# Kernel tuning notes

Hardware: AMD Instinct MI355X
Metric: run time of the kernel (lower is better)

The kernel has to match this reference:

```python
import jax, jax.numpy as jnp
import numpy as np

B, E, W, HID, HOR = 16, 128, 256, 64, 12
EPS = 1e-5


def conv1d(x, w, b, stride=1, padding=0, groups=1):
    # x: [N, Cin, L], w: [Cout, Cin//groups, K]
    y = jax.lax.conv_general_dilated(x, w, (stride,), [(padding, padding)],
                                     feature_group_count=groups,
                                     dimension_numbers=('NCH', 'OIH', 'NCH'))
    return y + b[None, :, None]


def setup_inputs() -> dict:
    key = jax.random.key(0)
    ks = jax.random.split(key, 20)
    def rn(k, shape, scale):
        return jax.random.normal(k, shape, dtype=jnp.float32) * scale
    return {
        'x': rn(ks[0], (B, 1, W), 1.0),
        'noise': rn(ks[1], (HOR, B * E), 1.0),
        'affine_weight': jnp.ones((E,), jnp.float32),
        'affine_bias': jnp.zeros((E,), jnp.float32),
        'pe_w1': rn(ks[2], (32, 1, 5), 1.0 / np.sqrt(5.0)),
        'pe_b1': jnp.zeros((32,), jnp.float32),
        'bn_gamma': jnp.ones((32,), jnp.float32),
        'bn_beta': jnp.zeros((32,), jnp.float32),
        'bn_mean': jnp.zeros((32,), jnp.float32),
        'bn_var': jnp.ones((32,), jnp.float32),
        'pe_w2': rn(ks[3], (E, 32, 1), 1.0 / np.sqrt(32.0)),
        'pe_b2': jnp.zeros((E,), jnp.float32),
        'net_w1': rn(ks[4], (E, 64, 1, 2), 1.0 / np.sqrt(2.0)),
        'net_b1': jnp.zeros((E, 64), jnp.float32),
        'net_w2': rn(ks[5], (E, 64, 4, 2), 1.0 / np.sqrt(8.0)),
        'net_b2': jnp.zeros((E, 64), jnp.float32),
        'net_w3': rn(ks[6], (E, 1, 64, 1), 1.0 / np.sqrt(64.0)),
        'net_b3': jnp.zeros((E, 1), jnp.float32),
        'gat_wl': rn(ks[7], (HID, HID), 1.0 / np.sqrt(HID)),
        'gat_bl': jnp.zeros((HID,), jnp.float32),
        'gat_wr': rn(ks[8], (HID, HID), 1.0 / np.sqrt(HID)),
        'gat_br': jnp.zeros((HID,), jnp.float32),
        'gat_attn': rn(ks[9], (HID,), 1.0 / np.sqrt(HID)),
        'out_w': rn(ks[10], (E, HID), 1.0 / np.sqrt(HID)),
        'out_b': jnp.zeros((E,), jnp.float32),
        'ce_w': rn(ks[11], (HID, 3), 1.0 / np.sqrt(3.0)),
        'ce_b': jnp.zeros((HID,), jnp.float32),
        'cd_w': rn(ks[12], (4, HID), 1.0 / np.sqrt(HID)),
        'cd_b': jnp.zeros((4,), jnp.float32),
        'q_w': rn(ks[13], (32, W), 1.0 / np.sqrt(W)),
        'q_b': jnp.zeros((32,), jnp.float32),
        'k_w': rn(ks[14], (32, W), 1.0 / np.sqrt(W)),
        'k_b': jnp.zeros((32,), jnp.float32),
    }


def reference(x, noise, affine_weight, affine_bias, pe_w1, pe_b1, bn_gamma, bn_beta,
              bn_mean, bn_var, pe_w2, pe_b2, net_w1, net_b1, net_w2, net_b2, net_w3,
              net_b3, gat_wl, gat_bl, gat_wr, gat_br, gat_attn, out_w, out_b,
              ce_w, ce_b, cd_w, cd_b, q_w, q_b, k_w, k_b):
    # instance norm over time axis (unbiased=False, no eps, as in the torch code)
    mean = jnp.mean(x, axis=2, keepdims=True)              # [B,1,1]
    std = jnp.sqrt(jnp.var(x, axis=2, keepdims=True))
    xn = (x - mean) / std

    # path_encoder: conv(1->32,k5,p2) + ReLU + BN(eval) + conv(32->E,k1)
    h0 = jax.nn.relu(conv1d(xn, pe_w1, pe_b1, padding=2))
    h0 = (h0 - bn_mean[None, :, None]) / jnp.sqrt(bn_var + EPS)[None, :, None]
    h0 = h0 * bn_gamma[None, :, None] + bn_beta[None, :, None]
    xf = conv1d(h0, pe_w2, pe_b2)                          # [B,E,W]
    xf = xf * affine_weight[None, :, None] + affine_bias[None, :, None]

    # adjacency learner: softmax(Q K^T) over nodes, then hard threshold
    q = jnp.einsum('bew,hw->beh', xf, q_w) + q_b           # [B,E,32]
    k = jnp.einsum('bew,hw->beh', xf, k_w) + k_b
    adj_soft = jax.nn.softmax(jnp.einsum('bih,bjh->bij', q, k), axis=-1)  # [B,E,E]
    adj_bin = (adj_soft > 0.5).astype(jnp.float32)

    def cnn1d(xc, w1, b1, w2, b2, w3, b3):
        # xc: [B,1,W] -> [B,1,HID]; kernel=stride=down_factor//2=2
        h1 = jnp.tanh(conv1d(xc, w1, b1, stride=2))
        h2 = jnp.tanh(conv1d(h1, w2, b2, stride=2, groups=16))
        return jnp.tanh(conv1d(h2, w3, b3))

    vcnn = jax.vmap(cnn1d, in_axes=(0, 0, 0, 0, 0, 0, 0))

    def gat(h, adj):
        # GATv2, single head, is_concat: e[b,i,j] = a^T lrelu(g_r[i]+g_l[j])
        gl = jnp.einsum('bnf,of->bno', h, gat_wl) + gat_bl   # [B,N,HID]
        gr = jnp.einsum('bnf,of->bno', h, gat_wr) + gat_br
        gs = gr[:, :, None, :] + gl[:, None, :, :]           # [B,N,N,HID]
        e = jnp.einsum('bijf,f->bij', jax.nn.leaky_relu(gs, 0.2), gat_attn)
        e = jnp.where(adj == 0, jnp.float32(-1e20), e)
        a = jax.nn.softmax(e, axis=2)
        return jnp.einsum('bij,bjf->bif', a, gr)             # [B,N,HID]

    def mech(Q_t, P_t, adj, nz):
        Hh, Ee, Vv = Q_t[:, 0], Q_t[:, 1], Q_t[:, 2]
        al, be, ga, et = P_t[:, 0], P_t[:, 1], P_t[:, 2], P_t[:, 3]
        E_coup = jnp.einsum('bij,bj->bi', adj, Ee.reshape(B, E)).reshape(B * E)
        H_new = Hh - al * Hh
        E_new = Ee + be * Hh - ga * Ee + 0.1 * E_coup
        V_new = Vv + et * Ee + nz * 0.01
        return jnp.stack([H_new, E_new, V_new], axis=1)

    Q0 = jnp.tile(jnp.array([1.0, 0.0, 0.0], jnp.float32), (B * E, 1))

    def step(carry, nz):
        xc, Q_t = carry
        xper = xc.transpose(1, 0, 2)[:, :, None, :]          # [E,B,1,W]
        h = vcnn(xper, net_w1, net_b1, net_w2, net_b2, net_w3, net_b3)
        h = h[:, :, 0, :].transpose(1, 0, 2)                 # [B,E,HID]
        h_temp = gat(h, adj_bin)
        H_causal = jnp.tanh(Q_t @ ce_w.T + ce_b).reshape(B, E, HID)
        h = h + jnp.tanh(h_temp) + H_causal
        x_pred = jnp.einsum('beh,eh->be', h, out_w) + out_b  # grouped conv == per-node dot
        x_new = jnp.concatenate([xc[:, :, 1:], x_pred[:, :, None]], axis=2)
        P_t = jax.nn.sigmoid(h.reshape(B * E, HID) @ cd_w.T + cd_b)
        Q_new = mech(Q_t, P_t, adj_bin, nz)
        return (x_new, Q_new), (x_pred, P_t)

    (_, Q_final), (x_preds, P_all) = jax.lax.scan(step, (xf, Q0), noise)
    x_pred_all = x_preds.transpose(1, 2, 0)                  # [B,E,HOR]
    out = (x_pred_all - affine_bias[None, :, None]) / affine_weight[None, :, None]
    out = out * std + mean
    return out, Q_final.reshape(B, E, 3), P_all[-1].reshape(B, E, 4), adj_soft
```

## Files before the change

kernel.cpp:

```cpp
#include <hip/hip_runtime.h>


typedef __attribute__((ext_vector_type(4))) float f32x4;

struct Params {
  const float *__restrict__ x, *__restrict__ noise, *__restrict__ aw, *__restrict__ ab,
              *__restrict__ pe_w1, *__restrict__ pe_b1, *__restrict__ bn_g, *__restrict__ bn_b,
              *__restrict__ bn_m, *__restrict__ bn_v, *__restrict__ pe_w2, *__restrict__ pe_b2,
              *__restrict__ w1, *__restrict__ b1, *__restrict__ w2, *__restrict__ b2,
              *__restrict__ w3, *__restrict__ b3, *__restrict__ wl, *__restrict__ bl,
              *__restrict__ wr, *__restrict__ br, *__restrict__ attn, *__restrict__ out_w,
              *__restrict__ out_b, *__restrict__ ce_w, *__restrict__ ce_b, *__restrict__ cd_w,
              *__restrict__ cd_b, *__restrict__ q_w, *__restrict__ q_b, *__restrict__ k_w,
              *__restrict__ k_b;
  float* ws;
  float* out;
};

__device__ __forceinline__ float fast_tanh(float x) {
  float t = exp2f(fminf(2.8853900818f * x, 126.0f));
  return 1.0f - 2.0f * __builtin_amdgcn_rcpf(t + 1.0f);
}
__device__ __forceinline__ float fast_sigmoid(float x) {
  float t = exp2f(fminf(-1.44269504f * x, 126.0f));
  return __builtin_amdgcn_rcpf(1.0f + t);
}
__device__ __forceinline__ float wsum(float v) {
  #pragma unroll
  for (int m = 1; m < 64; m <<= 1) v += __shfl_xor(v, m, 64);
  return v;
}
__device__ __forceinline__ float wmax(float v) {
  #pragma unroll
  for (int m = 1; m < 64; m <<= 1) v = fmaxf(v, __shfl_xor(v, m, 64));
  return v;
}
__device__ __forceinline__ float load_llc(const float* p) {
  return __hip_atomic_load(p, __ATOMIC_RELAXED, __HIP_MEMORY_SCOPE_AGENT);
}
__device__ __forceinline__ void store_llc(float* p, float v) {
  __hip_atomic_store(p, v, __ATOMIC_RELAXED, __HIP_MEMORY_SCOPE_AGENT);
}
__device__ __forceinline__ f32x4 load_llc4(const float* p) {
  f32x4 v;
  asm volatile("global_load_dwordx4 %0, %1, off sc0 sc1" : "=v"(v) : "v"(p));
  return v;
}
__device__ __forceinline__ unsigned to_bf16(float f) {
  unsigned u = __float_as_uint(f);
  return (u + 0x7fffu + ((u >> 16) & 1u)) >> 16;
}
__device__ __forceinline__ unsigned pk(float lo, float hi) {
  return to_bf16(lo) | (to_bf16(hi) << 16);
}
__device__ __forceinline__ float blo(unsigned w) { return __uint_as_float(w << 16); }
__device__ __forceinline__ float bhi(unsigned w) { return __uint_as_float(w & 0xffff0000u); }

#define OFF_MS   0
#define OFF_EB   32
#define OFF_CNT  4128
#define OFF_QV   16416
#define OFF_KV   81952
#define OFF_GL   147488
#define OFF_GR   409632
#define OFF_H0   671776
#define OFF_XW   802848
#define OFF_G    1359904
#define OFF_ADJ  1916960

__global__ __launch_bounds__(256)
void k1_h0(Params P) {
  __shared__ float red[8];
  const int tid = threadIdx.x, blk = blockIdx.x;
  const int idx = blk * 256 + tid;
  const int b = idx >> 13, c = (idx >> 8) & 31, w = idx & 255;
  const int lane = tid & 63, wv = tid >> 6;

  float v = P.x[b * 256 + w];
  float s = wsum(v), s2 = wsum(v * v);
  if (lane == 0) { red[wv] = s; red[4 + wv] = s2; }
  __syncthreads();
  float st  = red[0] + red[1] + red[2] + red[3];
  float st2 = red[4] + red[5] + red[6] + red[7];
  float mean = st * (1.f / 256.f);
  float var  = st2 * (1.f / 256.f) - mean * mean;
  float sd   = sqrtf(var);
  float* ms = P.ws + OFF_MS;
  if (tid == 0) { ms[b] = mean; ms[16 + b] = sd; }

  float rstd = 1.f / sd;
  float acc = P.pe_b1[c];
  #pragma unroll
  for (int k = 0; k < 5; k++) {
    int u = w - 2 + k;
    float xv = (u >= 0 && u < 256) ? (P.x[b * 256 + u] - mean) * rstd : 0.f;
    acc += P.pe_w1[c * 5 + k] * xv;
  }
  acc = fmaxf(acc, 0.f);
  float sc = P.bn_g[c] / sqrtf(P.bn_v[c] + 1e-5f);
  (P.ws + OFF_H0)[idx] = (acc - P.bn_m[c]) * sc + P.bn_b[c];
}

__global__ __launch_bounds__(256)
void k2_xf(Params P) {
  const int idx = blockIdx.x * 256 + threadIdx.x;
  const int b = idx >> 15, e = (idx >> 8) & 127, w = idx & 255;
  const float* w2p  = P.pe_w2 + e * 32;
  const float* hcol = P.ws + OFF_H0 + b * 8192 + w;
  float acc = P.pe_b2[e];
  #pragma unroll 8
  for (int c = 0; c < 32; c++) acc += w2p[c] * hcol[c * 256];
  acc = acc * P.aw[e] + P.ab[e];
  (P.ws + OFF_XW)[(b * 128 + e) * 272 + w] = acc;
}

__global__ __launch_bounds__(256)
void k34(Params P) {
  if (blockIdx.x < 2048) {
    const int row = blockIdx.x;
    const int es  = row & 127;
    const int s   = threadIdx.x;
    const float* w1p = P.w1 + es * 128;
    const float* w2p = P.w2 + es * 512;
    const float* w3p = P.w3 + es * 64;
    const float* b1p = P.b1 + es * 64;
    const float* b2p = P.b2 + es * 64;
    const float  b3v = P.b3[es];
    const float* xr  = P.ws + OFF_XW + row * 272;
    if (s >= 253) return;
    float X0 = xr[s], X1 = xr[s + 1], X2 = xr[s + 2], X3 = xr[s + 3];
    float acc = 0.f;
    #pragma unroll 1
    for (int g2 = 0; g2 < 16; g2++) {
      float h1v[8];
      #pragma unroll
      for (int ic = 0; ic < 4; ic++) {
        int ch = g2 * 4 + ic;
        float ww0 = w1p[ch * 2], ww1 = w1p[ch * 2 + 1], bb = b1p[ch];
        h1v[ic * 2 + 0] = fast_tanh(bb + ww0 * X0 + ww1 * X1);
        h1v[ic * 2 + 1] = fast_tanh(bb + ww0 * X2 + ww1 * X3);
      }
      #pragma unroll
      for (int oc = 0; oc < 4; oc++) {
        int ch = g2 * 4 + oc;
        const float* wq = w2p + ch * 8;
        float a2 = b2p[ch];
        #pragma unroll
        for (int u = 0; u < 8; u++) a2 += wq[u] * h1v[u];
        acc += w3p[ch] * fast_tanh(a2);
      }
    }
    (P.ws + OFF_G)[row * 272 + s] = fast_tanh(b3v + acc);
  } else {
    const int gtid = (blockIdx.x - 2048) * 256 + threadIdx.x;
    if (gtid < 16) ((int*)(P.ws + OFF_CNT))[gtid * 32] = 0;
    const int half = gtid >> 16;
    const int idx  = gtid & 65535;
    const int row  = idx >> 5, h = idx & 31;
    const float* wm  = half ? P.k_w : P.q_w;
    const float* bv  = half ? P.k_b : P.q_b;
    const float* xr  = P.ws + OFF_XW + row * 272;
    const float* wrw = wm + h * 256;
    float acc = bv[h];
    #pragma unroll 8
    for (int w = 0; w < 256; w += 4) {
      float4 xx = *(const float4*)(xr + w);
      float4 wq = *(const float4*)(wrw + w);
      acc += xx.x * wq.x + xx.y * wq.y + xx.z * wq.z + xx.w * wq.w;
    }
    ((half ? P.ws + OFF_KV : P.ws + OFF_QV))[idx] = acc;
  }
}

__global__ __launch_bounds__(256)
void k5_adj(Params P) {
  __shared__ __align__(16) float hbuf[4 * 64];
  const int tid = threadIdx.x, lane = tid & 63, wv = tid >> 6;
  const int row = blockIdx.x * 4 + wv;
  const int b = row >> 7;
  float* ws = P.ws;
  float* hb = hbuf + wv * 64;
  unsigned char* adjb = (unsigned char*)(ws + OFF_ADJ);

  if (lane < 32) hb[lane] = (ws + OFF_QV)[row * 32 + lane];
  __syncthreads();
  float ev0, ev1;
  #pragma unroll
  for (int half = 0; half < 2; half++) {
    int j = lane + half * 64;
    const float* kr = ws + OFF_KV + (b * 128 + j) * 32;
    float acc = 0.f;
    #pragma unroll
    for (int h = 0; h < 32; h += 4) {
      float4 kk = *(const float4*)(kr + h);
      float4 qq = *(const float4*)(hb + h);
      acc += qq.x * kk.x + qq.y * kk.y + qq.z * kk.z + qq.w * kk.w;
    }
    if (half == 0) ev0 = acc; else ev1 = acc;
  }
  float m   = wmax(fmaxf(ev0, ev1));
  float p0  = __expf(ev0 - m), p1 = __expf(ev1 - m);
  float inv = 1.f / wsum(p0 + p1);
  float a0 = p0 * inv, a1 = p1 * inv;
  P.out[38912 + row * 128 + lane]      = a0;
  P.out[38912 + row * 128 + lane + 64] = a1;
  adjb[row * 128 + lane]      = (a0 > 0.5f) ? 1 : 0;
  adjb[row * 128 + lane + 64] = (a1 > 0.5f) ? 1 : 0;
}

__global__ __launch_bounds__(1024, 4)
void k_scan(Params P) {
  __shared__ __align__(16) unsigned glS2_[4096];
  __shared__ __align__(16) unsigned grTS_[4096];
  __shared__ __align__(16) unsigned WS_[4096];
  __shared__ __align__(16) float wscb[16 * 336];
  __shared__ __align__(16) float attnS[64];
  const int tid = threadIdx.x, lane = tid & 63, wv = tid >> 6;
  const int row = blockIdx.x * 16 + wv;
  const int b = row >> 7, e = row & 127;
  float* ws = P.ws;
  float* abuf = wscb + wv * 336;
  float* hb   = abuf + 128;
  float* h1b  = abuf + 192;
  float* hist = abuf + 320;
  const float4* hb4   = (const float4*)hb;
  const float4* abuf4 = (const float4*)abuf;
  const float4* attn4 = (const float4*)attnS;
  char* glS  = (char*)glS2_;
  char* grTS = (char*)grTS_;
  char* WSc  = (char*)WS_;
  const float* grow_G = ws + OFF_G + row * 272;
  const unsigned char* arow = (const unsigned char*)(ws + OFF_ADJ) + row * 128;
  int* cntb = (int*)(ws + OFF_CNT) + b * 32;

  {
    int o = tid >> 4, c = tid & 15;
    float4 vl = *(const float4*)(P.wl + o * 64 + c * 4);
    float4 vr = *(const float4*)(P.wr + o * 64 + c * 4);
    uint4 u;
    u.x = pk(vl.x, vr.x); u.y = pk(vl.y, vr.y);
    u.z = pk(vl.z, vr.z); u.w = pk(vl.w, vr.w);
    *(uint4*)(WSc + o * 256 + ((c ^ (o & 15)) << 4)) = u;
  }
  if (tid < 64) attnS[tid] = P.attn[tid];

  float cew0 = P.ce_w[lane * 3], cew1 = P.ce_w[lane * 3 + 1], cew2 = P.ce_w[lane * 3 + 2];
  float cebv = P.ce_b[lane];
  float cdw0 = P.cd_w[lane], cdw1 = P.cd_w[64 + lane], cdw2 = P.cd_w[128 + lane], cdw3 = P.cd_w[192 + lane];
  float cdb0 = P.cd_b[0], cdb1 = P.cd_b[1], cdb2 = P.cd_b[2], cdb3 = P.cd_b[3];
  float outw = P.out_w[e * 64 + lane], outb = P.out_b[e];
  float blv = P.bl[lane], brv = P.br[lane];
  float awv = P.aw[e], abv = P.ab[e];
  float meanb = ws[OFF_MS + b], stdb = ws[OFF_MS + 16 + b];
  float w10 = P.w1[e * 128 + lane * 2], w11 = P.w1[e * 128 + lane * 2 + 1];
  float b1v = P.b1[e * 64 + lane], b2v = P.b2[e * 64 + lane];
  float w3v = P.w3[e * 64 + lane], b3c = P.b3[e];
  float w2r[8];
  {
    const float4* w24 = (const float4*)(P.w2 + e * 512 + lane * 8);
    float4 a = w24[0], c = w24[1];
    w2r[0] = a.x; w2r[1] = a.y; w2r[2] = a.z; w2r[3] = a.w;
    w2r[4] = c.x; w2r[5] = c.y; w2r[6] = c.z; w2r[7] = c.w;
  }
  const bool a0b = arow[lane] != 0, a1b = arow[lane + 64] != 0;
  float h_own = grow_G[4 * lane];
  float xA = (ws + OFF_XW)[row * 272 + 253];
  float xB = (ws + OFF_XW)[row * 272 + 254];
  float xC = (ws + OFF_XW)[row * 272 + 255];
  float q0 = 1.f, q1 = 0.f, q2 = 0.f;
  if (lane == 0) store_llc(ws + OFF_EB + row, 0.f);

  __syncthreads();

  hb[lane] = h_own;
  __syncthreads();
  float gri;
  {
    float glx = blv, grx = brv;
    const int k = lane & 15;
    #pragma unroll
    for (int q = 0; q < 16; q++) {
      float4 hq = hb4[q];
      uint4 w = *(const uint4*)(WSc + lane * 256 + ((q ^ k) << 4));
      glx += hq.x * blo(w.x) + hq.y * blo(w.y) + hq.z * blo(w.z) + hq.w * blo(w.w);
      grx += hq.x * bhi(w.x) + hq.y * bhi(w.y) + hq.z * bhi(w.z) + hq.w * bhi(w.w);
    }
    store_llc(ws + OFF_GL + row * 64 + lane, glx);
    store_llc(ws + OFF_GR + b * 8192 + lane * 128 + e, grx);
    gri = grx;
  }

  const int pp = tid >> 4, pc = tid & 15;
  const int ff = tid >> 4, fc = tid & 15;

  #pragma unroll 1
  for (int t = 0; t < 12; t++) {
    asm volatile("s_waitcnt vmcnt(0)" ::: "memory");
    __syncthreads();
    if (tid == 0) {
      __hip_atomic_fetch_add(cntb, 1, __ATOMIC_RELAXED, __HIP_MEMORY_SCOPE_AGENT);
      const int target = (t + 1) * 8;
      while (__hip_atomic_load(cntb, __ATOMIC_RELAXED, __HIP_MEMORY_SCOPE_AGENT) < target)
        __builtin_amdgcn_s_sleep(2);
    }
    __syncthreads();

    const float* glG   = ws + OFF_GL + (t & 1) * 131072 + b * 8192;
    const float* grTG  = ws + OFF_GR + (t & 1) * 131072 + b * 8192;
    const float* EbO   = ws + OFF_EB + (t & 1) * 2048;
    float*       EbN   = ws + OFF_EB + ((t + 1) & 1) * 2048;
    float*       glGn  = ws + OFF_GL + ((t + 1) & 1) * 131072;
    float*       grTGn = ws + OFF_GR + ((t + 1) & 1) * 131072;

    {
      f32x4 va = load_llc4(glG + pp * 64 + pc * 4);
      f32x4 vb = load_llc4(glG + (pp + 64) * 64 + pc * 4);
      f32x4 vc = load_llc4(grTG + ff * 128 + fc * 8);
      f32x4 vd = load_llc4(grTG + ff * 128 + fc * 8 + 4);
      asm volatile("s_waitcnt vmcnt(0)" ::: "memory");
      __builtin_amdgcn_sched_barrier(0);
      uint4 ug;
      ug.x = pk(va[0], vb[0]); ug.y = pk(va[1], vb[1]);
      ug.z = pk(va[2], vb[2]); ug.w = pk(va[3], vb[3]);
      *(uint4*)(glS + pp * 256 + ((pc ^ (pp & 15)) << 4)) = ug;
      uint4 ur;
      ur.x = pk(vc[0], vc[1]); ur.y = pk(vc[2], vc[3]);
      ur.z = pk(vd[0], vd[1]); ur.w = pk(vd[2], vd[3]);
      *(uint4*)(grTS + ff * 256 + ((fc ^ (ff & 15)) << 4)) = ur;
    }
    hb[lane] = gri;
    __syncthreads();

    float ev0 = 0.f, ev1 = 0.f;
    {
      const char* r0 = glS + lane * 256;
      const int k = lane & 15;
      #pragma unroll
      for (int c = 0; c < 16; c++) {
        float4 hq = hb4[c];
        float4 aq = attn4[c];
        uint4 g = *(const uint4*)(r0 + ((c ^ k) << 4));
        float v;
        v = hq.x + blo(g.x); ev0 += fmaxf(v, 0.2f * v) * aq.x;
        v = hq.x + bhi(g.x); ev1 += fmaxf(v, 0.2f * v) * aq.x;
        v = hq.y + blo(g.y); ev0 += fmaxf(v, 0.2f * v) * aq.y;
        v = hq.y + bhi(g.y); ev1 += fmaxf(v, 0.2f * v) * aq.y;
        v = hq.z + blo(g.z); ev0 += fmaxf(v, 0.2f * v) * aq.z;
        v = hq.z + bhi(g.z); ev1 += fmaxf(v, 0.2f * v) * aq.z;
        v = hq.w + blo(g.w); ev0 += fmaxf(v, 0.2f * v) * aq.w;
        v = hq.w + bhi(g.w); ev1 += fmaxf(v, 0.2f * v) * aq.w;
      }
    }
    ev0 = a0b ? ev0 : -1e20f;
    ev1 = a1b ? ev1 : -1e20f;
    float m   = wmax(fmaxf(ev0, ev1));
    float p0  = __expf(ev0 - m), p1 = __expf(ev1 - m);
    float inv = 1.f / wsum(p0 + p1);
    abuf[lane]      = p0 * inv;
    abuf[lane + 64] = p1 * inv;
    __syncthreads();

    float ht = 0.f;
    {
      const char* rr = grTS + lane * 256;
      const int k = lane & 15;
      #pragma unroll
      for (int c = 0; c < 16; c++) {
        float4 aA = abuf4[2 * c], aB = abuf4[2 * c + 1];
        uint4 g = *(const uint4*)(rr + ((c ^ k) << 4));
        ht += aA.x * blo(g.x) + aA.y * bhi(g.x) + aA.z * blo(g.y) + aA.w * bhi(g.y)
            + aB.x * blo(g.z) + aB.y * bhi(g.z) + aB.z * blo(g.w) + aB.w * bhi(g.w);
      }
    }

    float hc = fast_tanh(cebv + q0 * cew0 + q1 * cew1 + q2 * cew2);
    float hf = h_own + fast_tanh(ht) + hc;

    float xp = wsum(hf * outw) + outb;
    float d0 = wsum(hf * cdw0);
    float d1 = wsum(hf * cdw1);
    float d2 = wsum(hf * cdw2);
    float d3 = wsum(hf * cdw3);
    float al = fast_sigmoid(d0 + cdb0);
    float be = fast_sigmoid(d1 + cdb1);
    float ga = fast_sigmoid(d2 + cdb2);
    float et = fast_sigmoid(d3 + cdb3);

    float ec = 0.f;
    if (a0b) ec += load_llc(EbO + b * 128 + lane);
    if (a1b) ec += load_llc(EbO + b * 128 + lane + 64);
    ec = wsum(ec);

    float Hn = q0 - al * q0;
    float En = q1 + be * q0 - ga * q1 + 0.1f * ec;
    float Vn = q2 + et * q1 + P.noise[t * 2048 + row] * 0.01f;
    q0 = Hn; q1 = En; q2 = Vn;
    if (lane == 0) {
      store_llc(EbN + row, En);
      P.out[row * 12 + t] = (xp - abv) / awv * stdb + meanb;
      if (t == 11) {
        P.out[24576 + row * 3]     = Hn;
        P.out[24576 + row * 3 + 1] = En;
        P.out[24576 + row * 3 + 2] = Vn;
        P.out[30720 + row * 4]     = al;
        P.out[30720 + row * 4 + 1] = be;
        P.out[30720 + row * 4 + 2] = ga;
        P.out[30720 + row * 4 + 3] = et;
      }
    }

    if (t < 11) {
      float X0 = xA, X1 = xB, X2 = xC, X3 = xp;
      xA = xB; xB = xC; xC = xp;
      float h1a = fast_tanh(b1v + w10 * X0 + w11 * X1);
      float h1c = fast_tanh(b1v + w10 * X2 + w11 * X3);
      h1b[lane * 2]     = h1a;
      h1b[lane * 2 + 1] = h1c;
      __syncthreads();
      const float* h1g = h1b + (lane >> 2) * 8;
      float a2 = b2v;
      #pragma unroll
      for (int u = 0; u < 8; u++) a2 += w2r[u] * h1g[u];
      float h2v = fast_tanh(a2);
      float g3  = wsum(w3v * h2v);
      float Gn  = fast_tanh(b3c + g3);
      if (lane == 0) hist[t] = Gn;

      float hnext;
      if (lane == 63) {
        hnext = Gn;
      } else {
        int gi = (t + 1) + 4 * lane;
        hnext = (gi >= 253) ? hist[gi - 253] : grow_G[gi];
      }
      __syncthreads();
      hb[lane] = hnext;
      __syncthreads();
      float glx = blv, grx = brv;
      const int k = lane & 15;
      #pragma unroll
      for (int q = 0; q < 16; q++) {
        float4 hq = hb4[q];
        uint4 w = *(const uint4*)(WSc + lane * 256 + ((q ^ k) << 4));
        glx += hq.x * blo(w.x) + hq.y * blo(w.y) + hq.z * blo(w.z) + hq.w * blo(w.w);
        grx += hq.x * bhi(w.x) + hq.y * bhi(w.y) + hq.z * bhi(w.z) + hq.w * bhi(w.w);
      }
      store_llc(glGn + row * 64 + lane, glx);
      store_llc(grTGn + b * 8192 + lane * 128 + e, grx);
      gri = grx;
      h_own = hnext;
    }
  }
}

extern "C" void kernel_launch(void* const* d_in, const int* in_sizes, int n_in,
                              void* d_out, int out_size, void* d_ws, size_t ws_size,
                              hipStream_t stream) {
  Params p;
  p.x     = (const float*)d_in[0];  p.noise = (const float*)d_in[1];
  p.aw    = (const float*)d_in[2];  p.ab    = (const float*)d_in[3];
  p.pe_w1 = (const float*)d_in[4];  p.pe_b1 = (const float*)d_in[5];
  p.bn_g  = (const float*)d_in[6];  p.bn_b  = (const float*)d_in[7];
  p.bn_m  = (const float*)d_in[8];  p.bn_v  = (const float*)d_in[9];
  p.pe_w2 = (const float*)d_in[10]; p.pe_b2 = (const float*)d_in[11];
  p.w1    = (const float*)d_in[12]; p.b1    = (const float*)d_in[13];
  p.w2    = (const float*)d_in[14]; p.b2    = (const float*)d_in[15];
  p.w3    = (const float*)d_in[16]; p.b3    = (const float*)d_in[17];
  p.wl    = (const float*)d_in[18]; p.bl    = (const float*)d_in[19];
  p.wr    = (const float*)d_in[20]; p.br    = (const float*)d_in[21];
  p.attn  = (const float*)d_in[22]; p.out_w = (const float*)d_in[23];
  p.out_b = (const float*)d_in[24]; p.ce_w  = (const float*)d_in[25];
  p.ce_b  = (const float*)d_in[26]; p.cd_w  = (const float*)d_in[27];
  p.cd_b  = (const float*)d_in[28]; p.q_w   = (const float*)d_in[29];
  p.q_b   = (const float*)d_in[30]; p.k_w   = (const float*)d_in[31];
  p.k_b   = (const float*)d_in[32];
  p.ws  = (float*)d_ws;
  p.out = (float*)d_out;

  k1_h0<<<dim3(512),  dim3(256), 0, stream>>>(p);
  k2_xf<<<dim3(2048), dim3(256), 0, stream>>>(p);
  k34  <<<dim3(2560), dim3(256), 0, stream>>>(p);
  k5_adj<<<dim3(512), dim3(256), 0, stream>>>(p);
  k_scan<<<dim3(128), dim3(1024), 0, stream>>>(p);
}
```

Baseline: 250.6 us.

## Precompute static GAT projections per step and apply low-rank dynamic corrections in scan

Result: no change. 254.1 us (+1.4%).

```diff
diff --git a/kernel.cpp b/kernel.cpp
--- a/kernel.cpp
+++ b/kernel.cpp
@@ -46,6 +46,11 @@
   asm volatile("global_load_dwordx4 %0, %1, off sc0 sc1" : "=v"(v) : "v"(p));
   return v;
 }
+__device__ __forceinline__ float load_llc1(const float* p) {
+  float v;
+  asm volatile("global_load_dword %0, %1, off sc0 sc1" : "=v"(v) : "v"(p));
+  return v;
+}
 __device__ __forceinline__ unsigned to_bf16(float f) {
   unsigned u = __float_as_uint(f);
   return (u + 0x7fffu + ((u >> 16) & 1u)) >> 16;
@@ -67,6 +72,9 @@
 #define OFF_XW   802848
 #define OFF_G    1359904
 #define OFF_ADJ  1916960
+#define OFF_GDYN 1990688
+#define OFF_PNL  2015264
+#define WS_NEED_BYTES 14352512ull
 
 __global__ __launch_bounds__(256)
 void k1_h0(Params P) {
@@ -206,6 +214,307 @@
   P.out[38912 + row * 128 + lane + 64] = a1;
   adjb[row * 128 + lane]      = (a0 > 0.5f) ? 1 : 0;
   adjb[row * 128 + lane + 64] = (a1 > 0.5f) ? 1 : 0;
+}
+
+__global__ __launch_bounds__(1024)
+void k_pre(Params P) {
+  __shared__ __align__(16) unsigned WS_[4096];
+  __shared__ __align__(16) float hbb[16 * 128];
+  const int tid = threadIdx.x, lane = tid & 63, wv = tid >> 6;
+  char* WSc = (char*)WS_;
+  {
+    int o = tid >> 4, c = tid & 15;
+    float4 vl = *(const float4*)(P.wl + o * 64 + c * 4);
+    float4 vr = *(const float4*)(P.wr + o * 64 + c * 4);
+    uint4 u;
+    u.x = pk(vl.x, vr.x); u.y = pk(vl.y, vr.y);
+    u.z = pk(vl.z, vr.z); u.w = pk(vl.w, vr.w);
+    *(uint4*)(WSc + o * 256 + ((c ^ (o & 15)) << 4)) = u;
+  }
+  const int wid = blockIdx.x * 16 + wv;
+  const int t = wid >> 10, rem = wid & 1023, b = rem >> 6, p = rem & 63;
+  const int r0 = b * 128 + p, r1 = r0 + 64;
+  float* hb0 = hbb + wv * 128;
+  float* hb1 = hb0 + 64;
+  int gi = t + 4 * lane;
+  hb0[lane] = (gi < 253) ? (P.ws + OFF_G)[r0 * 272 + gi] : 0.f;
+  hb1[lane] = (gi < 253) ? (P.ws + OFF_G)[r1 * 272 + gi] : 0.f;
+  __syncthreads();
+  float gl0 = P.bl[lane], gr0 = P.br[lane];
+  float gl1 = gl0, gr1 = gr0;
+  const int k = lane & 15;
+  const float4* h04 = (const float4*)hb0;
+  const float4* h14 = (const float4*)hb1;
+  #pragma unroll
+  for (int q = 0; q < 16; q++) {
+    uint4 w = *(const uint4*)(WSc + lane * 256 + ((q ^ k) << 4));
+    float4 a = h04[q], c4 = h14[q];
+    gl0 += a.x * blo(w.x) + a.y * blo(w.y) + a.z * blo(w.z) + a.w * blo(w.w);
+    gr0 += a.x * bhi(w.x) + a.y * bhi(w.y) + a.z * bhi(w.z) + a.w * bhi(w.w);
+    gl1 += c4.x * blo(w.x) + c4.y * blo(w.y) + c4.z * blo(w.z) + c4.w * blo(w.w);
+    gr1 += c4.x * bhi(w.x) + c4.y * bhi(w.y) + c4.z * bhi(w.z) + c4.w * bhi(w.w);
+  }
+  unsigned* pnl = (unsigned*)(P.ws + OFF_PNL) + (t * 16 + b) * 8192;
+  pnl[p * 64 + lane]        = pk(gl0, gl1);
+  pnl[4096 + lane * 64 + p] = pk(gr0, gr1);
+}
+
+__global__ __launch_bounds__(1024, 4)
+void k_scan2(Params P) {
+  __shared__ __align__(16) unsigned glS2_[4096];
+  __shared__ __align__(16) unsigned grTS_[4096];
+  __shared__ __align__(16) unsigned WS_[4096];
+  __shared__ __align__(16) float gdS[512];
+  __shared__ __align__(16) float wscb[16 * 336];
+  __shared__ __align__(16) float attnS[64];
+  const int tid = threadIdx.x, lane = tid & 63, wv = tid >> 6;
+  const int row = blockIdx.x * 16 + wv;
+  const int b = row >> 7, e = row & 127;
+  float* ws = P.ws;
+  float* abuf = wscb + wv * 336;
+  float* hb   = abuf + 128;
+  float* h1b  = abuf + 192;
+  float* hist = abuf + 320;
+  const float4* hb4   = (const float4*)hb;
+  const float4* abuf4 = (const float4*)abuf;
+  const float4* attn4 = (const float4*)attnS;
+  char* glS  = (char*)glS2_;
+  char* grTS = (char*)grTS_;
+  char* WSc  = (char*)WS_;
+  const float* grow_G = ws + OFF_G + row * 272;
+  const unsigned char* arow = (const unsigned char*)(ws + OFF_ADJ) + row * 128;
+  int* cntb = (int*)(ws + OFF_CNT) + b * 32;
+
+  {
+    int o = tid >> 4, c = tid & 15;
+    float4 vl = *(const float4*)(P.wl + o * 64 + c * 4);
+    float4 vr = *(const float4*)(P.wr + o * 64 + c * 4);
+    uint4 u;
+    u.x = pk(vl.x, vr.x); u.y = pk(vl.y, vr.y);
+    u.z = pk(vl.z, vr.z); u.w = pk(vl.w, vr.w);
+    *(uint4*)(WSc + o * 256 + ((c ^ (o & 15)) << 4)) = u;
+  }
+  if (tid < 64) attnS[tid] = P.attn[tid];
+
+  float cew0 = P.ce_w[lane * 3], cew1 = P.ce_w[lane * 3 + 1], cew2 = P.ce_w[lane * 3 + 2];
+  float cebv = P.ce_b[lane];
+  float cdw0 = P.cd_w[lane], cdw1 = P.cd_w[64 + lane], cdw2 = P.cd_w[128 + lane], cdw3 = P.cd_w[192 + lane];
+  float cdb0 = P.cd_b[0], cdb1 = P.cd_b[1], cdb2 = P.cd_b[2], cdb3 = P.cd_b[3];
+  float outw = P.out_w[e * 64 + lane], outb = P.out_b[e];
+  float awv = P.aw[e], abv = P.ab[e];
+  float meanb = ws[OFF_MS + b], stdb = ws[OFF_MS + 16 + b];
+  float w10 = P.w1[e * 128 + lane * 2], w11 = P.w1[e * 128 + lane * 2 + 1];
+  float b1v = P.b1[e * 64 + lane], b2v = P.b2[e * 64 + lane];
+  float w3v = P.w3[e * 64 + lane], b3c = P.b3[e];
+  float w2r[8];
+  {
+    const float4* w24 = (const float4*)(P.w2 + e * 512 + lane * 8);
+    float4 a = w24[0], c = w24[1];
+    w2r[0] = a.x; w2r[1] = a.y; w2r[2] = a.z; w2r[3] = a.w;
+    w2r[4] = c.x; w2r[5] = c.y; w2r[6] = c.z; w2r[7] = c.w;
+  }
+  const bool a0b = arow[lane] != 0, a1b = arow[lane + 64] != 0;
+  float h_own = grow_G[4 * lane];
+  float xA = (ws + OFF_XW)[row * 272 + 253];
+  float xB = (ws + OFF_XW)[row * 272 + 254];
+  float xC = (ws + OFF_XW)[row * 272 + 255];
+  float q0 = 1.f, q1 = 0.f, q2 = 0.f;
+  if (lane == 0) store_llc(ws + OFF_EB + row, 0.f);
+
+  const int pp = tid >> 4, fc = tid & 15;
+  const int swk = pp & 15;
+
+  #pragma unroll 1
+  for (int t = 0; t < 12; t++) {
+    asm volatile("s_waitcnt vmcnt(0)" ::: "memory");
+    __syncthreads();
+    if (tid == 0) {
+      __hip_atomic_fetch_add(cntb, 1, __ATOMIC_RELAXED, __HIP_MEMORY_SCOPE_AGENT);
+      const int target = (t + 1) * 8;
+      while (__hip_atomic_load(cntb, __ATOMIC_RELAXED, __HIP_MEMORY_SCOPE_AGENT) < target)
+        __builtin_amdgcn_s_sleep(2);
+    }
+    __syncthreads();
+
+    const float* EbO = ws + OFF_EB + (t & 1) * 2048;
+    float*       EbN = ws + OFF_EB + ((t + 1) & 1) * 2048;
+    const int Nu = (t == 0) ? 0 : (t < 5) ? 1 : (t < 9) ? 2 : 3;
+
+    float ebv0 = load_llc1(EbO + b * 128 + lane);
+    float ebv1 = load_llc1(EbO + b * 128 + lane + 64);
+    f32x4 gdv;
+    const bool gdth = tid < Nu * 32;
+    if (gdth) {
+      int uk = tid >> 5;
+      int u  = (uk == 0) ? (t - 1) : (uk == 1) ? (t - 5) : (t - 9);
+      gdv = load_llc4(ws + OFF_GDYN + u * 2048 + b * 128 + (tid & 31) * 4);
+    }
+    const unsigned* pnl = (const unsigned*)(ws + OFF_PNL) + (t * 16 + b) * 8192;
+    uint4 vg = *(const uint4*)(pnl + pp * 64 + fc * 4);
+    uint4 vr = *(const uint4*)(pnl + 4096 + pp * 64 + fc * 4);
+    asm volatile("s_waitcnt vmcnt(0)" ::: "memory");
+    __builtin_amdgcn_sched_barrier(0);
+    if (gdth) *(f32x4*)(gdS + (tid >> 5) * 128 + (tid & 31) * 4) = gdv;
+    __syncthreads();
+
+    if (Nu) {
+      float g0[3], g1[3];
+      #pragma unroll
+      for (int kk = 0; kk < 3; kk++) if (kk < Nu) {
+        g0[kk] = gdS[kk * 128 + pp];
+        g1[kk] = gdS[kk * 128 + pp + 64];
+      }
+      unsigned* vgp = (unsigned*)&vg;
+      #pragma unroll
+      for (int i = 0; i < 4; i++) {
+        int o = fc * 4 + i;
+        float lo = blo(vgp[i]), hi = bhi(vgp[i]);
+        #pragma unroll
+        for (int kk = 0; kk < 3; kk++) if (kk < Nu) {
+          int fk = 63 - kk, cW = fk >> 2;
+          unsigned wv_ = *(const unsigned*)(WSc + o * 256 + ((cW ^ (o & 15)) << 4) + (fk & 3) * 4);
+          lo += g0[kk] * blo(wv_);
+          hi += g1[kk] * blo(wv_);
+        }
+        vgp[i] = pk(lo, hi);
+      }
+      float wrk[3];
+      #pragma unroll
+      for (int kk = 0; kk < 3; kk++) if (kk < Nu) {
+        int fk = 63 - kk, cW = fk >> 2;
+        unsigned wv_ = *(const unsigned*)(WSc + pp * 256 + ((cW ^ swk) << 4) + (fk & 3) * 4);
+        wrk[kk] = bhi(wv_);
+      }
+      unsigned* vrp = (unsigned*)&vr;
+      #pragma unroll
+      for (int i = 0; i < 4; i++) {
+        int p = fc * 4 + i;
+        float lo = blo(vrp[i]), hi = bhi(vrp[i]);
+        #pragma unroll
+        for (int kk = 0; kk < 3; kk++) if (kk < Nu) {
+          lo += gdS[kk * 128 + p] * wrk[kk];
+          hi += gdS[kk * 128 + p + 64] * wrk[kk];
+        }
+        vrp[i] = pk(lo, hi);
+      }
+    }
+    *(uint4*)(glS  + pp * 256 + ((fc ^ swk) << 4)) = vg;
+    *(uint4*)(grTS + pp * 256 + ((fc ^ swk) << 4)) = vr;
+    __syncthreads();
+
+    {
+      int pe = e & 63, cE = pe >> 2;
+      unsigned u = *(const unsigned*)(grTS + lane * 256 + ((cE ^ (lane & 15)) << 4) + (pe & 3) * 4);
+      hb[lane] = (e < 64) ? blo(u) : bhi(u);
+    }
+
+    float ev0 = 0.f, ev1 = 0.f;
+    {
+      const char* r0 = glS + lane * 256;
+      const int k = lane & 15;
+      #pragma unroll
+      for (int c = 0; c < 16; c++) {
+        float4 hq = hb4[c];
+        float4 aq = attn4[c];
+        uint4 g = *(const uint4*)(r0 + ((c ^ k) << 4));
+        float v;
+        v = hq.x + blo(g.x); ev0 += fmaxf(v, 0.2f * v) * aq.x;
+        v = hq.x + bhi(g.x); ev1 += fmaxf(v, 0.2f * v) * aq.x;
+        v = hq.y + blo(g.y); ev0 += fmaxf(v, 0.2f * v) * aq.y;
+        v = hq.y + bhi(g.y); ev1 += fmaxf(v, 0.2f * v) * aq.y;
+        v = hq.z + blo(g.z); ev0 += fmaxf(v, 0.2f * v) * aq.z;
+        v = hq.z + bhi(g.z); ev1 += fmaxf(v, 0.2f * v) * aq.z;
+        v = hq.w + blo(g.w); ev0 += fmaxf(v, 0.2f * v) * aq.w;
+        v = hq.w + bhi(g.w); ev1 += fmaxf(v, 0.2f * v) * aq.w;
+      }
+    }
+    ev0 = a0b ? ev0 : -1e20f;
+    ev1 = a1b ? ev1 : -1e20f;
+    float m   = wmax(fmaxf(ev0, ev1));
+    float p0  = __expf(ev0 - m), p1 = __expf(ev1 - m);
+    float inv = 1.f / wsum(p0 + p1);
+    abuf[lane]      = p0 * inv;
+    abuf[lane + 64] = p1 * inv;
+    __syncthreads();
+
+    float ht = 0.f;
+    {
+      const char* rr = grTS + lane * 256;
+      const int k = lane & 15;
+      #pragma unroll
+      for (int c = 0; c < 16; c++) {
+        float4 aA = abuf4[c];
+        float4 aB = abuf4[c + 16];
+        uint4 g = *(const uint4*)(rr + ((c ^ k) << 4));
+        ht += aA.x * blo(g.x) + aB.x * bhi(g.x) + aA.y * blo(g.y) + aB.y * bhi(g.y)
+            + aA.z * blo(g.z) + aB.z * bhi(g.z) + aA.w * blo(g.w) + aB.w * bhi(g.w);
+      }
+    }
+
+    float hc = fast_tanh(cebv + q0 * cew0 + q1 * cew1 + q2 * cew2);
+    float hf = h_own + fast_tanh(ht) + hc;
+
+    float xp = wsum(hf * outw) + outb;
+    float d0 = wsum(hf * cdw0);
+    float d1 = wsum(hf * cdw1);
+    float d2 = wsum(hf * cdw2);
+    float d3 = wsum(hf * cdw3);
+    float al = fast_sigmoid(d0 + cdb0);
+    float be = fast_sigmoid(d1 + cdb1);
+    float ga = fast_sigmoid(d2 + cdb2);
+    float et = fast_sigmoid(d3 + cdb3);
+
+    float ec = (a0b ? ebv0 : 0.f) + (a1b ? ebv1 : 0.f);
+    ec = wsum(ec);
+
+    float Hn = q0 - al * q0;
+    float En = q1 + be * q0 - ga * q1 + 0.1f * ec;
+    float Vn = q2 + et * q1 + P.noise[t * 2048 + row] * 0.01f;
+    q0 = Hn; q1 = En; q2 = Vn;
+    if (lane == 0) {
+      store_llc(EbN + row, En);
+      P.out[row * 12 + t] = (xp - abv) / awv * stdb + meanb;
+      if (t == 11) {
+        P.out[24576 + row * 3]     = Hn;
+        P.out[24576 + row * 3 + 1] = En;
+        P.out[24576 + row * 3 + 2] = Vn;
+        P.out[30720 + row * 4]     = al;
+        P.out[30720 + row * 4 + 1] = be;
+        P.out[30720 + row * 4 + 2] = ga;
+        P.out[30720 + row * 4 + 3] = et;
+      }
+    }
+
+    if (t < 11) {
+      float X0 = xA, X1 = xB, X2 = xC, X3 = xp;
+      xA = xB; xB = xC; xC = xp;
+      float h1a = fast_tanh(b1v + w10 * X0 + w11 * X1);
+      float h1c = fast_tanh(b1v + w10 * X2 + w11 * X3);
+      h1b[lane * 2]     = h1a;
+      h1b[lane * 2 + 1] = h1c;
+      __syncthreads();
+      const float* h1g = h1b + (lane >> 2) * 8;
+      float a2 = b2v;
+      #pragma unroll
+      for (int u = 0; u < 8; u++) a2 += w2r[u] * h1g[u];
+      float h2v = fast_tanh(a2);
+      float g3  = wsum(w3v * h2v);
+      float Gn  = fast_tanh(b3c + g3);
+      if (lane == 0) {
+        hist[t] = Gn;
+        store_llc(ws + OFF_GDYN + t * 2048 + row, Gn);
+      }
+      float hnext;
+      if (lane == 63) {
+        hnext = Gn;
+      } else {
+        int gi = (t + 1) + 4 * lane;
+        hnext = (gi >= 253) ? hist[gi - 253] : grow_G[gi];
+      }
+      __syncthreads();
+      h_own = hnext;
+    }
+  }
 }
 
 __global__ __launch_bounds__(1024, 4)
@@ -481,5 +790,10 @@
   k2_xf<<<dim3(2048), dim3(256), 0, stream>>>(p);
   k34  <<<dim3(2560), dim3(256), 0, stream>>>(p);
   k5_adj<<<dim3(512), dim3(256), 0, stream>>>(p);
-  k_scan<<<dim3(128), dim3(1024), 0, stream>>>(p);
-}
+  if (ws_size >= WS_NEED_BYTES + 65536) {
+    k_pre  <<<dim3(768), dim3(1024), 0, stream>>>(p);
+    k_scan2<<<dim3(128), dim3(1024), 0, stream>>>(p);
+  } else {
+    k_scan <<<dim3(128), dim3(1024), 0, stream>>>(p);
+  }
+}
```
